# Kernel optimization log

Measured on AMD Instinct MI355X. Metric: run time of the kernel, lower is better.

## Reference

```python
import jax, jax.numpy as jnp
import numpy as np

B, T, C, H = 8, 1024, 768, 12
HD = C // H  # 64


def setup_inputs() -> dict:
    key = jax.random.key(0)
    ks = jax.random.split(key, 9)
    s = 0.02
    x = jax.random.normal(ks[0], (B, T, C), dtype=jnp.float32)
    mask = jnp.tril(jnp.ones((T, T), dtype=bool))[None, None, :, :]  # causal [1,1,T,T]
    wq = jax.random.normal(ks[1], (C, C), dtype=jnp.float32) * s
    wk = jax.random.normal(ks[2], (C, C), dtype=jnp.float32) * s
    wv = jax.random.normal(ks[3], (C, C), dtype=jnp.float32) * s
    wo = jax.random.normal(ks[4], (C, C), dtype=jnp.float32) * s
    bq = jnp.zeros((C,), dtype=jnp.float32)
    bk = jnp.zeros((C,), dtype=jnp.float32)
    bv = jnp.zeros((C,), dtype=jnp.float32)
    bo = jnp.zeros((C,), dtype=jnp.float32)
    return {"x": x, "mask": mask, "wq": wq, "bq": bq, "wk": wk, "bk": bk,
            "wv": wv, "bv": bv, "wo": wo, "bo": bo}


def reference(x, mask, wq, bq, wk, bk, wv, bv, wo, bo):
    Bx, Tx, Cx = x.shape
    # QKV projections (flax Dense: y = x @ W + b)
    q = (x @ wq + bq).reshape(Bx, Tx, H, HD).transpose(0, 2, 1, 3)  # [B,H,T,hd]
    k = (x @ wk + bk).reshape(Bx, Tx, H, HD).transpose(0, 2, 1, 3)
    v = (x @ wv + bv).reshape(Bx, Tx, H, HD).transpose(0, 2, 1, 3)
    attn = jnp.einsum('bhtd,bhsd->bhts', q, k) / jnp.sqrt(jnp.float32(HD))
    attn = jnp.where(mask, attn, jnp.float32(-1e9))
    attn = jax.nn.softmax(attn, axis=-1)
    out = jnp.einsum('bhts,bhsd->bhtd', attn, v)  # [B,H,T,hd]
    out = out.transpose(0, 2, 1, 3).reshape(Bx, Tx, Cx)
    return out @ wo + bo
```

## Files before the change

kernel.cpp:

```cpp
#include <hip/hip_runtime.h>
#include <hip/hip_bf16.h>

typedef __bf16 bf16_t;
typedef __bf16 bf16x8 __attribute__((ext_vector_type(8)));
typedef float f32x4 __attribute__((ext_vector_type(4)));

#define NB 8
#define NT 1024
#define NC 768
#define NH 12
#define NHD 64

__device__ __forceinline__ f32x4 mfma16(bf16x8 a, bf16x8 b, f32x4 c) {
  return __builtin_amdgcn_mfma_f32_16x16x32_bf16(a, b, c, 0, 0, 0);
}

__device__ __forceinline__ void gld_lds16(const void* g, void* l) {
  __builtin_amdgcn_global_load_lds((const __attribute__((address_space(1))) void*)g,
                                   (__attribute__((address_space(3))) void*)l, 16, 0, 0);
}

__global__ void cvt_x(const float* __restrict__ in, bf16_t* __restrict__ out, int n4) {
  int i = blockIdx.x * blockDim.x + threadIdx.x;
  if (i >= n4) return;
  float4 v = ((const float4*)in)[i];
  bf16_t o[4] = {(bf16_t)v.x, (bf16_t)v.y, (bf16_t)v.z, (bf16_t)v.w};
  *(uint2*)(out + i * 4) = *(uint2*)o;
}

__global__ void transpose_w(const float* __restrict__ wq, const float* __restrict__ wk,
                            const float* __restrict__ wv, const float* __restrict__ wo,
                            bf16_t* __restrict__ wqkvT, bf16_t* __restrict__ woT) {
  __shared__ float tile[32][33];
  const int m = blockIdx.z;
  const float* in = (m == 0) ? wq : (m == 1) ? wk : (m == 2) ? wv : wo;
  bf16_t* out = (m == 3) ? woT : (wqkvT + m * NC * NC);
  const int tx = threadIdx.x & 31, ty = threadIdx.x >> 5;
  const int x = blockIdx.x * 32 + tx;
  const int y0 = blockIdx.y * 32;
#pragma unroll
  for (int i = 0; i < 32; i += 8)
    tile[ty + i][tx] = in[(size_t)(y0 + ty + i) * NC + x];
  __syncthreads();
  const int ox = y0 + tx;
  const int oy0 = blockIdx.x * 32;
#pragma unroll
  for (int i = 0; i < 32; i += 8)
    out[(size_t)(oy0 + ty + i) * NC + ox] = (bf16_t)tile[tx][ty + i];
}

__global__ void transpose_v(const bf16_t* __restrict__ V, bf16_t* __restrict__ VT) {
  __shared__ bf16_t tile[32][33];
  const int bh = blockIdx.z;
  const int x0 = blockIdx.x * 32;
  const int y0 = blockIdx.y * 32;
  const int tx = threadIdx.x & 31, ty = threadIdx.x >> 5;
  const bf16_t* in = V + (size_t)bh * NT * NHD;
  bf16_t* out = VT + (size_t)bh * NHD * NT;
#pragma unroll
  for (int i = 0; i < 32; i += 8)
    tile[ty + i][tx] = in[(size_t)(y0 + ty + i) * NHD + x0 + tx];
  __syncthreads();
#pragma unroll
  for (int i = 0; i < 32; i += 8)
    out[(size_t)(x0 + ty + i) * NT + y0 + tx] = tile[tx][ty + i];
}

template <int MODE, int BM>
__global__ __launch_bounds__(256) void gemm_t(
    const bf16_t* __restrict__ A, const bf16_t* __restrict__ BT, int K,
    const float* __restrict__ b0, const float* __restrict__ b1,
    const float* __restrict__ b2, float* __restrict__ outF,
    bf16_t* __restrict__ out0, bf16_t* __restrict__ out1,
    bf16_t* __restrict__ out2) {
  constexpr int NJ = (BM == 128) ? 4 : 2;
  __shared__ __align__(16) bf16_t lA[2][BM * 32];
  __shared__ __align__(16) bf16_t lB[2][128 * 32];
  const int tid = threadIdx.x;
  const int lane = tid & 63, wave = tid >> 6;
  const int quad = lane >> 4, l16 = lane & 15;
  const int bm = blockIdx.x * BM, bn = blockIdx.y * 128;
  const int wm = (BM == 128) ? (wave >> 1) * 64 : 0;
  const int wn = (BM == 128) ? (wave & 1) * 64 : wave * 32;

  const int ra = tid >> 2;
  const int cc = tid & 3;
  const int kca = cc ^ ((ra >> 1) & 3);

  f32x4 acc[4][4] = {};

  const bf16_t* Ar = A + (size_t)(bm + ra) * K + kca * 8;
  const bf16_t* Ar2 = A + (size_t)(bm + 64 + ra) * K + kca * 8;
  const bf16_t* Br = BT + (size_t)(bn + ra) * K + kca * 8;
  const bf16_t* Br2 = BT + (size_t)(bn + 64 + ra) * K + kca * 8;

#define GSTAGE(K0, BUF)                                       \
  do {                                                        \
    char* lAb_ = (char*)lA[BUF] + wave * 1024;                \
    char* lBb_ = (char*)lB[BUF] + wave * 1024;                \
    gld_lds16(Ar + (K0), lAb_);                               \
    if (BM == 128) gld_lds16(Ar2 + (K0), lAb_ + 4096);        \
    gld_lds16(Br + (K0), lBb_);                               \
    gld_lds16(Br2 + (K0), lBb_ + 4096);                       \
  } while (0)

  GSTAGE(0, 0);

  for (int k0 = 0, it = 0; k0 < K; k0 += 32, ++it) {
    const int cur = it & 1;
    __syncthreads();
    if (k0 + 32 < K) GSTAGE(k0 + 32, cur ^ 1);
    const char* lAb = (const char*)lA[cur];
    const char* lBb = (const char*)lB[cur];

    bf16x8 af[4], bfr[NJ];
#pragma unroll
    for (int i = 0; i < 4; i++) {
      int row = wm + i * 16 + l16;
      int ch = quad ^ ((row >> 1) & 3);
      af[i] = *(const bf16x8*)(lAb + row * 64 + ch * 16);
    }
#pragma unroll
    for (int j = 0; j < NJ; j++) {
      int row = wn + j * 16 + l16;
      int ch = quad ^ ((row >> 1) & 3);
      bfr[j] = *(const bf16x8*)(lBb + row * 64 + ch * 16);
    }
    if (MODE == 0) {
#pragma unroll
      for (int j = 0; j < NJ; j++)
#pragma unroll
        for (int i = 0; i < 4; i++)
          acc[j][i] = mfma16(bfr[j], af[i], acc[j][i]);
    } else {
#pragma unroll
      for (int i = 0; i < 4; i++)
#pragma unroll
        for (int j = 0; j < NJ; j++)
          acc[i][j] = mfma16(af[i], bfr[j], acc[i][j]);
    }
  }
#undef GSTAGE

  if (MODE == 0) {
#pragma unroll
    for (int j = 0; j < NJ; j++) {
      int n0 = bn + wn + j * 16 + quad * 4;
      float4 b4 = *(const float4*)(b0 + n0);
      float bb4[4] = {b4.x, b4.y, b4.z, b4.w};
#pragma unroll
      for (int i = 0; i < 4; i++) {
        int m = bm + wm + i * 16 + l16;
        float4 o;
        o.x = acc[j][i][0] + bb4[0];
        o.y = acc[j][i][1] + bb4[1];
        o.z = acc[j][i][2] + bb4[2];
        o.w = acc[j][i][3] + bb4[3];
        *(float4*)(outF + (size_t)m * NC + n0) = o;
      }
    }
  } else {
#pragma unroll
    for (int j = 0; j < NJ; j++) {
      int n = bn + wn + j * 16 + l16;
      int sel = n / 768;
      int nl = n - sel * 768;
      int h = nl >> 6, d = nl & 63;
      const float* bp = (sel == 0) ? b0 : (sel == 1) ? b1 : b2;
      bf16_t* dst = (sel == 0) ? out0 : (sel == 1) ? out1 : out2;
      float bias = bp[nl];
      float scl = (sel == 0) ? 0.125f : 1.0f;
#pragma unroll
      for (int i = 0; i < 4; i++) {
        int m0 = bm + wm + i * 16 + quad * 4;
#pragma unroll
        for (int r = 0; r < 4; r++) {
          int m = m0 + r;
          int bb = m >> 10, t = m & 1023;
          dst[((size_t)(bb * NH + h) * NT + t) * NHD + d] =
              (bf16_t)((acc[i][j][r] + bias) * scl);
        }
      }
    }
  }
}

__global__ __launch_bounds__(256) void attn_fwd(
    const bf16_t* __restrict__ Q, const bf16_t* __restrict__ Kt,
    const bf16_t* __restrict__ VT, bf16_t* __restrict__ AO) {
  __shared__ __align__(16) bf16_t lK[2][64 * 64];
  __shared__ __align__(16) bf16_t lV[2][64 * 64];
  __shared__ __align__(16) bf16_t lP[8][16 * 72];
  const int tid = threadIdx.x, lane = tid & 63, wave = tid >> 6;
  const int quad = lane >> 4, l16 = lane & 15;
  const int bh = blockIdx.x;
  const int bx = blockIdx.y;
  const int b = bh / NH, h = bh - b * NH;
  const int qtA = bx, qtB = 15 - bx;
  const int jmax = qtB;

  const size_t qbase = (size_t)bh * NT;
  const size_t qoffA = (qbase + qtA * 64 + wave * 16 + l16) * NHD;
  const size_t qoffB = (qbase + qtB * 64 + wave * 16 + l16) * NHD;
  const bf16x8 aqA0 = *(const bf16x8*)(Q + qoffA + quad * 8);
  const bf16x8 aqA1 = *(const bf16x8*)(Q + qoffA + 32 + quad * 8);
  const bf16x8 aqB0 = *(const bf16x8*)(Q + qoffB + quad * 8);
  const bf16x8 aqB1 = *(const bf16x8*)(Q + qoffB + 32 + quad * 8);

  f32x4 lsA = {0.f, 0.f, 0.f, 0.f}, lsB = lsA;
  f32x4 OfA[4] = {}, OfB[4] = {};
  const f32x4 zero = {0.f, 0.f, 0.f, 0.f};

  const int sr = tid >> 3;
  const int sc = (tid & 7) ^ (sr & 7);
  const bf16_t* Kg0 = Kt + qbase * NHD;
  const bf16_t* Vg0 = VT + (size_t)bh * 64 * NT;
  const size_t kO0 = (size_t)sr * 64 + sc * 8, kO1 = kO0 + (size_t)32 * 64;
  const size_t vO0 = (size_t)sr * NT + sc * 8, vO1 = vO0 + (size_t)32 * NT;

  bf16_t* lPA = lP[wave * 2 + 0];
  bf16_t* lPB = lP[wave * 2 + 1];
  const int sb = quad ^ (l16 >> 2);

#define STAGE(JT, BUF)                                                  \
  do {                                                                  \
    const bf16_t* Kg_ = Kg0 + (size_t)(JT) * 64 * NHD;                  \
    const bf16_t* Vg_ = Vg0 + (JT) * 64;                                \
    char* dK_ = (char*)lK[BUF] + wave * 1024;                           \
    char* dV_ = (char*)lV[BUF] + wave * 1024;                           \
    gld_lds16(Kg_ + kO0, dK_);                                          \
    gld_lds16(Kg_ + kO1, dK_ + 4096);                                   \
    gld_lds16(Vg_ + vO0, dV_);                                          \
    gld_lds16(Vg_ + vO1, dV_ + 4096);                                   \
  } while (0)

  STAGE(0, 0);

  for (int j = 0; j <= jmax; ++j) {
    const int cur = j & 1;
    __syncthreads();
    if (j < jmax) STAGE(j + 1, cur ^ 1);
    const bf16_t* lKc = lK[cur];
    const bf16_t* lVc = lV[cur];
    const bool actA = (j <= qtA);

    f32x4 sA[4], sB[4];
#pragma unroll
    for (int nn = 0; nn < 4; nn++) {
      int row = nn * 16 + l16;
      int sw = row & 7;
      bf16x8 k0 = *(const bf16x8*)((char*)lKc + row * 128 + (quad ^ sw) * 16);
      bf16x8 k1 = *(const bf16x8*)((char*)lKc + row * 128 + ((quad + 4) ^ sw) * 16);
      sB[nn] = mfma16(aqB0, k0, zero);
      sB[nn] = mfma16(aqB1, k1, sB[nn]);
      if (actA) {
        sA[nn] = mfma16(aqA0, k0, zero);
        sA[nn] = mfma16(aqA1, k1, sA[nn]);
      }
    }

    if (j == qtB) {
#pragma unroll
      for (int nn = 0; nn < 4; nn++) {
        int key = nn * 16 + l16;
#pragma unroll
        for (int r = 0; r < 4; r++) {
          int qrow = wave * 16 + quad * 4 + r;
          if (key > qrow) sB[nn][r] = -1e30f;
        }
      }
    }
    if (actA && j == qtA) {
#pragma unroll
      for (int nn = 0; nn < 4; nn++) {
        int key = nn * 16 + l16;
#pragma unroll
        for (int r = 0; r < 4; r++) {
          int qrow = wave * 16 + quad * 4 + r;
          if (key > qrow) sA[nn][r] = -1e30f;
        }
      }
    }

#pragma unroll
    for (int nn = 0; nn < 4; nn++)
#pragma unroll
      for (int r = 0; r < 4; r++) {
        float pv = __expf(sB[nn][r]);
        lsB[r] += pv;
        lPB[(quad * 4 + r) * 72 + ((nn * 16 + l16) ^ (quad * 8))] = (bf16_t)pv;
      }
    if (actA) {
#pragma unroll
      for (int nn = 0; nn < 4; nn++)
#pragma unroll
        for (int r = 0; r < 4; r++) {
          float pv = __expf(sA[nn][r]);
          lsA[r] += pv;
          lPA[(quad * 4 + r) * 72 + ((nn * 16 + l16) ^ (quad * 8))] = (bf16_t)pv;
        }
    }
    asm volatile("s_waitcnt lgkmcnt(0)" ::: "memory");

    const bf16x8 apB0 = *(const bf16x8*)(lPB + l16 * 72 + sb * 8);
    const bf16x8 apB1 = *(const bf16x8*)(lPB + l16 * 72 + (sb + 4) * 8);
    bf16x8 apA0, apA1;
    if (actA) {
      apA0 = *(const bf16x8*)(lPA + l16 * 72 + sb * 8);
      apA1 = *(const bf16x8*)(lPA + l16 * 72 + (sb + 4) * 8);
    }
#pragma unroll
    for (int dd = 0; dd < 4; dd++) {
      int row = dd * 16 + l16;
      int sw = row & 7;
      bf16x8 v0 = *(const bf16x8*)((char*)lVc + row * 128 + (quad ^ sw) * 16);
      bf16x8 v1 = *(const bf16x8*)((char*)lVc + row * 128 + ((quad + 4) ^ sw) * 16);
      OfB[dd] = mfma16(apB0, v0, OfB[dd]);
      OfB[dd] = mfma16(apB1, v1, OfB[dd]);
      if (actA) {
        OfA[dd] = mfma16(apA0, v0, OfA[dd]);
        OfA[dd] = mfma16(apA1, v1, OfA[dd]);
      }
    }
  }
#undef STAGE

#pragma unroll
  for (int off = 8; off >= 1; off >>= 1)
#pragma unroll
    for (int r = 0; r < 4; r++) {
      lsA[r] += __shfl_xor(lsA[r], off, 64);
      lsB[r] += __shfl_xor(lsB[r], off, 64);
    }

#pragma unroll
  for (int g = 0; g < 2; g++) {
    f32x4* Of = g ? OfB : OfA;
    f32x4& lrun = g ? lsB : lsA;
    const int qt = g ? qtB : qtA;
    f32x4 inv;
#pragma unroll
    for (int r = 0; r < 4; r++) inv[r] = 1.0f / lrun[r];
    const int tq = qt * 64 + wave * 16 + quad * 4;
#pragma unroll
    for (int dd = 0; dd < 4; dd++) {
      int col = h * 64 + dd * 16 + l16;
#pragma unroll
      for (int r = 0; r < 4; r++)
        AO[((size_t)b * NT + tq + r) * NC + col] = (bf16_t)(Of[dd][r] * inv[r]);
    }
  }
}

extern "C" void kernel_launch(void* const* d_in, const int* in_sizes, int n_in,
                              void* d_out, int out_size, void* d_ws, size_t ws_size,
                              hipStream_t stream) {
  const float* x = (const float*)d_in[0];
  const float* wq = (const float*)d_in[2];
  const float* bq = (const float*)d_in[3];
  const float* wk = (const float*)d_in[4];
  const float* bk = (const float*)d_in[5];
  const float* wv = (const float*)d_in[6];
  const float* bv = (const float*)d_in[7];
  const float* wo = (const float*)d_in[8];
  const float* bo = (const float*)d_in[9];

  float* outF = (float*)d_out;
  bf16_t* Qb = (bf16_t*)d_out;
  bf16_t* Vb = Qb + (size_t)NB * NH * NT * NHD;
  bf16_t* ws = (bf16_t*)d_ws;
  bf16_t* xb = ws;
  bf16_t* wqkvT = xb + (size_t)NB * NT * NC;
  bf16_t* woT = wqkvT + (size_t)2304 * 768;
  bf16_t* Kb = woT + (size_t)768 * 768;
  bf16_t* VTb = Kb + (size_t)NB * NH * NT * NHD;
  bf16_t* AO = VTb + (size_t)NB * NH * NT * NHD;

  const int n4 = NB * NT * NC / 4;
  cvt_x<<<(n4 + 255) / 256, 256, 0, stream>>>(x, xb, n4);
  transpose_w<<<dim3(24, 24, 4), 256, 0, stream>>>(wq, wk, wv, wo, wqkvT, woT);
  gemm_t<1, 128><<<dim3(64, 18), 256, 0, stream>>>(xb, wqkvT, NC, bq, bk, bv,
                                                   nullptr, Qb, Kb, Vb);
  transpose_v<<<dim3(2, 32, 96), 256, 0, stream>>>(Vb, VTb);
  attn_fwd<<<dim3(96, 8), 256, 0, stream>>>(Qb, Kb, VTb, AO);
  gemm_t<0, 64><<<dim3(128, 6), 256, 0, stream>>>(AO, woT, NC, bo, nullptr, nullptr,
                                                  outF, nullptr, nullptr, nullptr);
}
```

Baseline: 199.2 us.

## Merge x conversion into weight prep kernel and deepen output GEMM K-tile

Folds the fp32-to-bf16 conversion of x into the weight transpose kernel as an extra grid slice, which removes one launch. The output projection GEMM is split into a dedicated kernel that stages K in chunks of 64 instead of 32, with a new XOR swizzle, halving the number of barrier iterations. The cost is more LDS per block for the output GEMM. The conversion now runs on only 576 blocks through a grid-stride loop, which may lower its parallelism.

```diff
diff --git a/kernel.cpp b/kernel.cpp
--- a/kernel.cpp
+++ b/kernel.cpp
@@ -20,27 +20,30 @@
                                    (__attribute__((address_space(3))) void*)l, 16, 0, 0);
 }
 
-__global__ void cvt_x(const float* __restrict__ in, bf16_t* __restrict__ out, int n4) {
-  int i = blockIdx.x * blockDim.x + threadIdx.x;
-  if (i >= n4) return;
-  float4 v = ((const float4*)in)[i];
-  bf16_t o[4] = {(bf16_t)v.x, (bf16_t)v.y, (bf16_t)v.z, (bf16_t)v.w};
-  *(uint2*)(out + i * 4) = *(uint2*)o;
-}
-
-__global__ void transpose_w(const float* __restrict__ wq, const float* __restrict__ wk,
-                            const float* __restrict__ wv, const float* __restrict__ wo,
-                            bf16_t* __restrict__ wqkvT, bf16_t* __restrict__ woT) {
+__global__ void prep(const float* __restrict__ x, bf16_t* __restrict__ xb,
+                     const float* __restrict__ wq, const float* __restrict__ wk,
+                     const float* __restrict__ wv, const float* __restrict__ wo,
+                     bf16_t* __restrict__ wqkvT, bf16_t* __restrict__ woT) {
+  const int m = blockIdx.z;
+  if (m == 4) {
+    const int n4 = NB * NT * NC / 4;
+    int i = (blockIdx.y * 24 + blockIdx.x) * 256 + threadIdx.x;
+    for (; i < n4; i += 24 * 24 * 256) {
+      float4 v = ((const float4*)x)[i];
+      bf16_t o[4] = {(bf16_t)v.x, (bf16_t)v.y, (bf16_t)v.z, (bf16_t)v.w};
+      *(uint2*)(xb + i * 4) = *(uint2*)o;
+    }
+    return;
+  }
   __shared__ float tile[32][33];
-  const int m = blockIdx.z;
   const float* in = (m == 0) ? wq : (m == 1) ? wk : (m == 2) ? wv : wo;
   bf16_t* out = (m == 3) ? woT : (wqkvT + m * NC * NC);
   const int tx = threadIdx.x & 31, ty = threadIdx.x >> 5;
-  const int x = blockIdx.x * 32 + tx;
+  const int xx = blockIdx.x * 32 + tx;
   const int y0 = blockIdx.y * 32;
 #pragma unroll
   for (int i = 0; i < 32; i += 8)
-    tile[ty + i][tx] = in[(size_t)(y0 + ty + i) * NC + x];
+    tile[ty + i][tx] = in[(size_t)(y0 + ty + i) * NC + xx];
   __syncthreads();
   const int ox = y0 + tx;
   const int oy0 = blockIdx.x * 32;
@@ -66,22 +69,18 @@
     out[(size_t)(x0 + ty + i) * NT + y0 + tx] = tile[tx][ty + i];
 }
 
-template <int MODE, int BM>
-__global__ __launch_bounds__(256) void gemm_t(
+__global__ __launch_bounds__(256) void gemm_qkv(
     const bf16_t* __restrict__ A, const bf16_t* __restrict__ BT, int K,
     const float* __restrict__ b0, const float* __restrict__ b1,
-    const float* __restrict__ b2, float* __restrict__ outF,
-    bf16_t* __restrict__ out0, bf16_t* __restrict__ out1,
-    bf16_t* __restrict__ out2) {
-  constexpr int NJ = (BM == 128) ? 4 : 2;
-  __shared__ __align__(16) bf16_t lA[2][BM * 32];
+    const float* __restrict__ b2, bf16_t* __restrict__ out0,
+    bf16_t* __restrict__ out1, bf16_t* __restrict__ out2) {
+  __shared__ __align__(16) bf16_t lA[2][128 * 32];
   __shared__ __align__(16) bf16_t lB[2][128 * 32];
   const int tid = threadIdx.x;
   const int lane = tid & 63, wave = tid >> 6;
   const int quad = lane >> 4, l16 = lane & 15;
-  const int bm = blockIdx.x * BM, bn = blockIdx.y * 128;
-  const int wm = (BM == 128) ? (wave >> 1) * 64 : 0;
-  const int wn = (BM == 128) ? (wave & 1) * 64 : wave * 32;
+  const int bm = blockIdx.x * 128, bn = blockIdx.y * 128;
+  const int wm = (wave >> 1) * 64, wn = (wave & 1) * 64;
 
   const int ra = tid >> 2;
   const int cc = tid & 3;
@@ -99,7 +98,7 @@
     char* lAb_ = (char*)lA[BUF] + wave * 1024;                \
     char* lBb_ = (char*)lB[BUF] + wave * 1024;                \
     gld_lds16(Ar + (K0), lAb_);                               \
-    if (BM == 128) gld_lds16(Ar2 + (K0), lAb_ + 4096);        \
+    gld_lds16(Ar2 + (K0), lAb_ + 4096);                       \
     gld_lds16(Br + (K0), lBb_);                               \
     gld_lds16(Br2 + (K0), lBb_ + 4096);                       \
   } while (0)
@@ -113,7 +112,7 @@
     const char* lAb = (const char*)lA[cur];
     const char* lBb = (const char*)lB[cur];
 
-    bf16x8 af[4], bfr[NJ];
+    bf16x8 af[4], bfr[4];
 #pragma unroll
     for (int i = 0; i < 4; i++) {
       int row = wm + i * 16 + l16;
@@ -121,66 +120,118 @@
       af[i] = *(const bf16x8*)(lAb + row * 64 + ch * 16);
     }
 #pragma unroll
-    for (int j = 0; j < NJ; j++) {
+    for (int j = 0; j < 4; j++) {
       int row = wn + j * 16 + l16;
       int ch = quad ^ ((row >> 1) & 3);
       bfr[j] = *(const bf16x8*)(lBb + row * 64 + ch * 16);
     }
-    if (MODE == 0) {
-#pragma unroll
-      for (int j = 0; j < NJ; j++)
+#pragma unroll
+    for (int i = 0; i < 4; i++)
+#pragma unroll
+      for (int j = 0; j < 4; j++)
+        acc[i][j] = mfma16(af[i], bfr[j], acc[i][j]);
+  }
+#undef GSTAGE
+
+#pragma unroll
+  for (int j = 0; j < 4; j++) {
+    int n = bn + wn + j * 16 + l16;
+    int sel = n / 768;
+    int nl = n - sel * 768;
+    int h = nl >> 6, d = nl & 63;
+    const float* bp = (sel == 0) ? b0 : (sel == 1) ? b1 : b2;
+    bf16_t* dst = (sel == 0) ? out0 : (sel == 1) ? out1 : out2;
+    float bias = bp[nl];
+    float scl = (sel == 0) ? 0.125f : 1.0f;
+#pragma unroll
+    for (int i = 0; i < 4; i++) {
+      int m0 = bm + wm + i * 16 + quad * 4;
+#pragma unroll
+      for (int r = 0; r < 4; r++) {
+        int m = m0 + r;
+        int bb = m >> 10, t = m & 1023;
+        dst[((size_t)(bb * NH + h) * NT + t) * NHD + d] =
+            (bf16_t)((acc[i][j][r] + bias) * scl);
+      }
+    }
+  }
+}
+
+__global__ __launch_bounds__(256) void gemm_o64(
+    const bf16_t* __restrict__ A, const bf16_t* __restrict__ BT,
+    const float* __restrict__ b0, float* __restrict__ outF) {
+  __shared__ __align__(16) bf16_t lA[2][64 * 64];
+  __shared__ __align__(16) bf16_t lB[2][128 * 64];
+  const int K = NC;
+  const int tid = threadIdx.x;
+  const int lane = tid & 63, wave = tid >> 6;
+  const int quad = lane >> 4, l16 = lane & 15;
+  const int bm = blockIdx.x * 64, bn = blockIdx.y * 128;
+  const int wn = wave * 32;
+
+  const int lr = lane >> 3;
+  const int sc = (lane & 7) ^ lr;
+  const bf16_t* Ar = A + (size_t)(bm + wave * 8 + lr) * K + sc * 8;
+  const bf16_t* Br = BT + (size_t)(bn + wave * 8 + lr) * K + sc * 8;
+
+  f32x4 acc[2][4] = {};
+
+#define OSTAGE(K0, BUF)                                  \
+  do {                                                   \
+    char* dA_ = (char*)lA[BUF] + wave * 1024;            \
+    char* dB_ = (char*)lB[BUF] + wave * 1024;            \
+    gld_lds16(Ar + (K0), dA_);                           \
+    gld_lds16(Ar + 32 * K + (K0), dA_ + 4096);           \
+    gld_lds16(Br + (K0), dB_);                           \
+    gld_lds16(Br + 32 * K + (K0), dB_ + 4096);           \
+    gld_lds16(Br + 64 * K + (K0), dB_ + 8192);           \
+    gld_lds16(Br + 96 * K + (K0), dB_ + 12288);          \
+  } while (0)
+
+  OSTAGE(0, 0);
+
+  for (int k0 = 0, it = 0; k0 < K; k0 += 64, ++it) {
+    const int cur = it & 1;
+    __syncthreads();
+    if (k0 + 64 < K) OSTAGE(k0 + 64, cur ^ 1);
+    const char* pA = (const char*)lA[cur];
+    const char* pB = (const char*)lB[cur];
+    const int sw = l16 & 7;
+#pragma unroll
+    for (int kk = 0; kk < 2; kk++) {
+      bf16x8 af[4], bfr[2];
+#pragma unroll
+      for (int i = 0; i < 4; i++) {
+        int row = i * 16 + l16;
+        af[i] = *(const bf16x8*)(pA + row * 128 + ((kk * 4 + quad) ^ sw) * 16);
+      }
+#pragma unroll
+      for (int j = 0; j < 2; j++) {
+        int row = wn + j * 16 + l16;
+        bfr[j] = *(const bf16x8*)(pB + row * 128 + ((kk * 4 + quad) ^ sw) * 16);
+      }
+#pragma unroll
+      for (int j = 0; j < 2; j++)
 #pragma unroll
         for (int i = 0; i < 4; i++)
           acc[j][i] = mfma16(bfr[j], af[i], acc[j][i]);
-    } else {
-#pragma unroll
-      for (int i = 0; i < 4; i++)
-#pragma unroll
-        for (int j = 0; j < NJ; j++)
-          acc[i][j] = mfma16(af[i], bfr[j], acc[i][j]);
-    }
-  }
-#undef GSTAGE
-
-  if (MODE == 0) {
-#pragma unroll
-    for (int j = 0; j < NJ; j++) {
-      int n0 = bn + wn + j * 16 + quad * 4;
-      float4 b4 = *(const float4*)(b0 + n0);
-      float bb4[4] = {b4.x, b4.y, b4.z, b4.w};
-#pragma unroll
-      for (int i = 0; i < 4; i++) {
-        int m = bm + wm + i * 16 + l16;
-        float4 o;
-        o.x = acc[j][i][0] + bb4[0];
-        o.y = acc[j][i][1] + bb4[1];
-        o.z = acc[j][i][2] + bb4[2];
-        o.w = acc[j][i][3] + bb4[3];
-        *(float4*)(outF + (size_t)m * NC + n0) = o;
-      }
-    }
-  } else {
-#pragma unroll
-    for (int j = 0; j < NJ; j++) {
-      int n = bn + wn + j * 16 + l16;
-      int sel = n / 768;
-      int nl = n - sel * 768;
-      int h = nl >> 6, d = nl & 63;
-      const float* bp = (sel == 0) ? b0 : (sel == 1) ? b1 : b2;
-      bf16_t* dst = (sel == 0) ? out0 : (sel == 1) ? out1 : out2;
-      float bias = bp[nl];
-      float scl = (sel == 0) ? 0.125f : 1.0f;
-#pragma unroll
-      for (int i = 0; i < 4; i++) {
-        int m0 = bm + wm + i * 16 + quad * 4;
-#pragma unroll
-        for (int r = 0; r < 4; r++) {
-          int m = m0 + r;
-          int bb = m >> 10, t = m & 1023;
-          dst[((size_t)(bb * NH + h) * NT + t) * NHD + d] =
-              (bf16_t)((acc[i][j][r] + bias) * scl);
-        }
-      }
+    }
+  }
+#undef OSTAGE
+
+#pragma unroll
+  for (int j = 0; j < 2; j++) {
+    int n0 = bn + wn + j * 16 + quad * 4;
+    float4 b4 = *(const float4*)(b0 + n0);
+#pragma unroll
+    for (int i = 0; i < 4; i++) {
+      int m = bm + i * 16 + l16;
+      float4 o;
+      o.x = acc[j][i][0] + b4.x;
+      o.y = acc[j][i][1] + b4.y;
+      o.z = acc[j][i][2] + b4.z;
+      o.w = acc[j][i][3] + b4.w;
+      *(float4*)(outF + (size_t)m * NC + n0) = o;
     }
   }
 }
@@ -376,13 +427,9 @@
   bf16_t* VTb = Kb + (size_t)NB * NH * NT * NHD;
   bf16_t* AO = VTb + (size_t)NB * NH * NT * NHD;
 
-  const int n4 = NB * NT * NC / 4;
-  cvt_x<<<(n4 + 255) / 256, 256, 0, stream>>>(x, xb, n4);
-  transpose_w<<<dim3(24, 24, 4), 256, 0, stream>>>(wq, wk, wv, wo, wqkvT, woT);
-  gemm_t<1, 128><<<dim3(64, 18), 256, 0, stream>>>(xb, wqkvT, NC, bq, bk, bv,
-                                                   nullptr, Qb, Kb, Vb);
+  prep<<<dim3(24, 24, 5), 256, 0, stream>>>(x, xb, wq, wk, wv, wo, wqkvT, woT);
+  gemm_qkv<<<dim3(64, 18), 256, 0, stream>>>(xb, wqkvT, NC, bq, bk, bv, Qb, Kb, Vb);
   transpose_v<<<dim3(2, 32, 96), 256, 0, stream>>>(Vb, VTb);
   attn_fwd<<<dim3(96, 8), 256, 0, stream>>>(Qb, Kb, VTb, AO);
-  gemm_t<0, 64><<<dim3(128, 6), 256, 0, stream>>>(AO, woT, NC, bo, nullptr, nullptr,
-                                                  outF, nullptr, nullptr, nullptr);
-}
+  gemm_o64<<<dim3(128, 6), 256, 0, stream>>>(AO, woT, bo, outF);
+}
```

New measurement: 194.5 us. -2.3%, faster.
